# Kernel optimization log

Hardware: AMD Instinct MI355X
Metric: run time of the kernel (lower is better)

The kernel has to match this reference:

```python
import jax, jax.numpy as jnp
import numpy as np

K_SIZE = 3
NUM_HEADS = 8
DIM = 128        # per-head feature dim
R = 128          # sketch dim
BATCH = 2
LENGTH = 2048
OUT_DIM = DIM * NUM_HEADS


def _conv1d(x, w, b=None):
    # x: [B, Cin, L], w: [Cout, Cin, K]
    y = jax.lax.conv_general_dilated(x, w, window_strides=(1,), padding='VALID',
                                     dimension_numbers=('NCH', 'OIH', 'NCH'))
    if b is not None:
        y = y + b[None, :, None]
    return y


def _sketch(x, g1, g2):
    # p == 2 branch: Sx = sqrt(r) * tanh((x@G1)*(x@G2)/sqrt(r))
    sqrt_r = jnp.asarray(np.sqrt(R), x.dtype)
    return sqrt_r * jnp.tanh((x @ g1) * (x @ g2) / sqrt_r)


def setup_inputs() -> dict:
    key = jax.random.key(0)
    ks = jax.random.split(key, 12)
    inp = {
        'x': jax.random.normal(ks[0], (BATCH, DIM, LENGTH), jnp.float32),
        'q_w': jax.random.normal(ks[1], (OUT_DIM, DIM, K_SIZE), jnp.float32) * (1.0 / np.sqrt(DIM * K_SIZE)),
        'q_b': jnp.zeros((OUT_DIM,), jnp.float32),
        'k_w': jax.random.normal(ks[2], (OUT_DIM, DIM, K_SIZE), jnp.float32) * (1.0 / np.sqrt(DIM * K_SIZE)),
        'k_b': jnp.zeros((OUT_DIM,), jnp.float32),
        'v_w': jax.random.normal(ks[3], (OUT_DIM, DIM, 1), jnp.float32) * (1.0 / np.sqrt(DIM)),
        'g1_q': jax.random.normal(ks[4], (DIM, R), jnp.float32) * (1.0 / np.sqrt(R)),
        'g2_q': jax.random.normal(ks[5], (DIM, R), jnp.float32) * (1.0 / np.sqrt(R)),
        'g1_k': jax.random.normal(ks[6], (DIM, R), jnp.float32) * (1.0 / np.sqrt(R)),
        'g2_k': jax.random.normal(ks[7], (DIM, R), jnp.float32) * (1.0 / np.sqrt(R)),
        'gamma_q': jnp.ones((1,), jnp.float32),
        'beta_q': jnp.zeros((1,), jnp.float32),
        'gamma_k': jnp.ones((1,), jnp.float32),
        'beta_k': jnp.zeros((1,), jnp.float32),
        'proj_w': jax.random.normal(ks[8], (DIM, OUT_DIM), jnp.float32) * (1.0 / np.sqrt(OUT_DIM)),
        'proj_b': jnp.zeros((DIM,), jnp.float32),
    }
    return inp


def reference(x, q_w, q_b, k_w, k_b, v_w, g1_q, g2_q, g1_k, g2_k,
              gamma_q, beta_q, gamma_k, beta_k, proj_w, proj_b):
    B, D, L = x.shape
    H = NUM_HEADS
    # causal left pad, then conv1d QKV projections
    x_pad = jnp.pad(x, ((0, 0), (0, 0), (K_SIZE - 1, 0)))
    q = _conv1d(x_pad, q_w, q_b)   # [B, H*D, L]
    k = _conv1d(x_pad, k_w, k_b)
    v = _conv1d(x, v_w)            # kernel size 1, no bias

    def shape(t):  # [B, H*D, L] -> [B, H, L, D]
        return t.reshape(B, H, D, L).transpose(0, 1, 3, 2)

    q, k, v = shape(q), shape(k), shape(v)
    q = gamma_q * q + beta_q
    k = gamma_k * k + beta_k
    phi_q = _sketch(q, g1_q, g2_q)  # [B, H, L, R]
    phi_k = _sketch(k, g1_k, g2_k)
    scores = jnp.einsum('bhlr,bhmr->bhlm', phi_q, phi_k)  # [B, H, L, L]
    attn = scores / (jnp.sum(scores, axis=-1, keepdims=True) + 1e-6)
    o = jnp.einsum('bhlm,bhmd->bhld', attn, v)            # [B, H, L, D]
    o = o.transpose(0, 1, 3, 2).reshape(B, H * D, L).transpose(0, 2, 1)  # [B, L, H*D]
    return o @ proj_w.T + proj_b
```

## Files before the change

kernel.cpp:

```cpp
#include <hip/hip_runtime.h>
#include <math.h>

#define BB 2
#define DD 128
#define LL 2048
#define HH 8
#define OC 1024
#define RR_ 128
#define BL (BB*LL)
#define NROW (BL*HH)
#define XROWS 2052


typedef __bf16  bf16x8  __attribute__((ext_vector_type(8)));
typedef float   float4v __attribute__((ext_vector_type(4)));

__device__ __forceinline__ void enc2(const float* src, bf16x8& p1, bf16x8& p2) {
    #pragma unroll
    for (int j = 0; j < 8; ++j) {
        float v = src[j];
        __bf16 h1 = (__bf16)v;
        p1[j] = h1;
        p2[j] = (__bf16)(v - (float)h1);
    }
}

__device__ __forceinline__ float fast_phi(double u1, double u2) {
    const double TWO_ISR = 0.17677669529663688110;
    const double LOG2E   = 1.44269504088896340736;
    const double SR      = 11.313708498984760390;
    double y = (u1*u2) * (TWO_ISR * LOG2E);
    y = fmin(fmax(y, -1020.4), 1020.4);
    double n = rint(y);
    double f = y - n;
    float ff = (float)f;
    float q;
    q = fmaf(1.01780860092396960e-7f, ff, 1.32154867901443094e-6f);
    q = fmaf(q, ff, 1.52527338040598403e-5f);
    q = fmaf(q, ff, 1.54035303933816099e-4f);
    q = fmaf(q, ff, 1.33335581464284434e-3f);
    q = fmaf(q, ff, 9.61812910762847716e-3f);
    q = fmaf(q, ff, 5.55041086648215800e-2f);
    double t2   = fma(f, (double)q, 0.24022650695910071233);
    double head = fma(f, 0.69314718055994530942, 1.0);
    double E0   = fma(f*f, t2, head);
    int ni = (int)n;
    double En = __hiloint2double((ni + 1023) << 20, 0);
    double E  = E0 * En;
    double den = E + 1.0;
    double r = (double)__builtin_amdgcn_rcpf((float)den);
    r = r * fma(-den, r, 2.0);
    r = r * fma(-den, r, 2.0);
    double t = fma(-2.0, r, 1.0);
    return (float)(SR * t);
}

__global__ __launch_bounds__(256) void enc_fused_k(
    const float* __restrict__ q_w, const float* __restrict__ k_w,
    const float* __restrict__ v_w, const float* __restrict__ pw,
    const float* __restrict__ g1_q, const float* __restrict__ g2_q,
    const float* __restrict__ g1_k, const float* __restrict__ g2_k,
    const float* __restrict__ x,
    __bf16* __restrict__ wenc, __bf16* __restrict__ genc,
    __bf16* __restrict__ venc, __bf16* __restrict__ penc,
    __bf16* __restrict__ xenc)
{
    __shared__ float t[32][33];
    const int bid = blockIdx.x;
    const int tid = threadIdx.x;
    if (bid < 2304) {
        const int gid = bid*256 + tid;
        if (gid < 262144) {
            const int o = gid >> 7, c = gid & 127;
            #pragma unroll
            for (int tt = 0; tt < 3; ++tt) {
                float v = (o < 1024) ? q_w[(o*128 + c)*3 + tt]
                                     : k_w[((o-1024)*128 + c)*3 + tt];
                __bf16 h1 = (__bf16)v;  float r1 = v - (float)h1;
                __bf16 h2 = (__bf16)r1; float r2 = r1 - (float)h2;
                __bf16 h3 = (__bf16)r2;
                wenc[((size_t)(0*3 + tt)*2048 + o)*128 + c] = h1;
                wenc[((size_t)(1*3 + tt)*2048 + o)*128 + c] = h2;
                wenc[((size_t)(2*3 + tt)*2048 + o)*128 + c] = h3;
            }
        } else if (gid < 262144 + 65536) {
            const int g = gid - 262144;
            const int mat = g >> 14, rem = g & 16383;
            const int r = rem >> 7, d = rem & 127;
            const float* src = (mat == 0) ? g1_q : (mat == 1) ? g2_q
                             : (mat == 2) ? g1_k : g2_k;
            float v = src[d*RR_ + r];
            __bf16 h1 = (__bf16)v;  float r1 = v - (float)h1;
            __bf16 h2 = (__bf16)r1; float r2 = r1 - (float)h2;
            __bf16 h3 = (__bf16)r2;
            genc[((size_t)(mat*3 + 0)*128 + r)*128 + d] = h1;
            genc[((size_t)(mat*3 + 1)*128 + r)*128 + d] = h2;
            genc[((size_t)(mat*3 + 2)*128 + r)*128 + d] = h3;
        } else if (gid < 262144 + 65536 + 131072) {
            const int g = gid - 262144 - 65536;
            const int o = g >> 7, c = g & 127;
            float v = v_w[o*128 + c];
            __bf16 h1 = (__bf16)v;  float r1 = v - (float)h1;
            __bf16 h2 = (__bf16)r1;
            venc[((size_t)0*1024 + o)*128 + c] = h1;
            venc[((size_t)1*1024 + o)*128 + c] = h2;
        } else if (gid < 262144 + 65536 + 131072 + 131072) {
            const int g = gid - 262144 - 65536 - 131072;
            const int j = g >> 10, k = g & 1023;
            float v = pw[(size_t)j*OC + k];
            __bf16 h1 = (__bf16)v;  float r1 = v - (float)h1;
            __bf16 h2 = (__bf16)r1;
            penc[((size_t)(0*128 + j))*OC + k] = h1;
            penc[((size_t)(1*128 + j))*OC + k] = h2;
        }
    } else {
        const int g = bid - 2304;
        const int lt = g & 63, ct = (g >> 6) & 3, b = g >> 8;
        const int l0 = lt*32, c0 = ct*32;
        for (int e = tid; e < 32*32; e += 256) {
            int c = e >> 5, l = e & 31;
            t[c][l] = x[((size_t)(b*DD + c0 + c))*LL + l0 + l];
        }
        __syncthreads();
        for (int e = tid; e < 32*32; e += 256) {
            int l = e >> 5, c = e & 31;
            float v = t[c][l];
            __bf16 h1 = (__bf16)v;  float r1 = v - (float)h1;
            __bf16 h2 = (__bf16)r1; float r2 = r1 - (float)h2;
            __bf16 h3 = (__bf16)r2;
            const size_t row = (size_t)(l0 + l + 2);
            xenc[((size_t)(0*2 + b)*XROWS + row)*128 + c0 + c] = h1;
            xenc[((size_t)(1*2 + b)*XROWS + row)*128 + c0 + c] = h2;
            xenc[((size_t)(2*2 + b)*XROWS + row)*128 + c0 + c] = h3;
        }
        if (lt == 0 && ct == 0) {
            for (int e = tid; e < 2*128; e += 256) {
                int row = e >> 7, c = e & 127;
                xenc[((size_t)(0*2 + b)*XROWS + row)*128 + c] = (__bf16)0.f;
                xenc[((size_t)(1*2 + b)*XROWS + row)*128 + c] = (__bf16)0.f;
                xenc[((size_t)(2*2 + b)*XROWS + row)*128 + c] = (__bf16)0.f;
            }
        }
    }
}

__global__ __launch_bounds__(256, 3) void conv_mfma_k(
    const __bf16* __restrict__ xenc, const __bf16* __restrict__ wenc,
    const __bf16* __restrict__ venc,
    const float* __restrict__ q_b, const float* __restrict__ k_b,
    const float* __restrict__ gamma_q, const float* __restrict__ beta_q,
    const float* __restrict__ gamma_k, const float* __restrict__ beta_k,
    float* __restrict__ q_s, float* __restrict__ k_s, float* __restrict__ v_s)
{
    __shared__ __bf16 As[3][66][136];
    const int tid  = threadIdx.x;
    const int wave = tid >> 6;
    const int lane = tid & 63;
    const int m    = lane & 15;
    const int quad = lane >> 4;
    const int bx = blockIdx.x;
    const int b  = bx >> 5;
    const int lb0 = (bx & 31) << 6;
    const int yt = blockIdx.y;

    for (int e = tid; e < 3*66*16; e += 256) {
        const int p = e / (66*16), rem = e % (66*16);
        const int row = rem >> 4, cg = rem & 15;
        *(bf16x8*)&As[p][row][cg*8] =
            *(const bf16x8*)&xenc[((size_t)(p*2 + b)*XROWS + lb0 + row)*128 + cg*8];
    }
    __syncthreads();

    if (yt < 32) {
        const int o0 = yt << 6;
        const int osub = o0 + wave*16;
        float4v corr[4][2];
        float4v accm[4];
        double  s64[4][4];
        #pragma unroll
        for (int lt = 0; lt < 4; ++lt) {
            corr[lt][0] = (float4v){0.f,0.f,0.f,0.f};
            corr[lt][1] = (float4v){0.f,0.f,0.f,0.f};
            #pragma unroll
            for (int reg = 0; reg < 4; ++reg) s64[lt][reg] = 0.0;
        }
        #pragma unroll
        for (int cidx = 0; cidx < 4; ++cidx) {
            const int c0 = cidx << 5;
            #pragma unroll
            for (int lt = 0; lt < 4; ++lt) accm[lt] = (float4v){0.f,0.f,0.f,0.f};
            #pragma unroll
            for (int t = 0; t < 3; ++t) {
                size_t base = ((size_t)t*2048 + osub + m)*128 + c0 + quad*8;
                bf16x8 B1 = *(const bf16x8*)&wenc[base];
                bf16x8 B2 = *(const bf16x8*)&wenc[base + (size_t)3*2048*128];
                bf16x8 B3 = *(const bf16x8*)&wenc[base + (size_t)6*2048*128];
                #pragma unroll
                for (int lt = 0; lt < 4; ++lt) {
                    const int row = lt*16 + m + t;
                    bf16x8 A1 = *(const bf16x8*)&As[0][row][c0 + quad*8];
                    bf16x8 A2 = *(const bf16x8*)&As[1][row][c0 + quad*8];
                    bf16x8 A3 = *(const bf16x8*)&As[2][row][c0 + quad*8];
                    accm[lt]    = __builtin_amdgcn_mfma_f32_16x16x32_bf16(A1, B1, accm[lt], 0, 0, 0);
                    corr[lt][0] = __builtin_amdgcn_mfma_f32_16x16x32_bf16(A1, B2, corr[lt][0], 0, 0, 0);
                    corr[lt][1] = __builtin_amdgcn_mfma_f32_16x16x32_bf16(A2, B1, corr[lt][1], 0, 0, 0);
                    corr[lt][0] = __builtin_amdgcn_mfma_f32_16x16x32_bf16(A1, B3, corr[lt][0], 0, 0, 0);
                    corr[lt][1] = __builtin_amdgcn_mfma_f32_16x16x32_bf16(A3, B1, corr[lt][1], 0, 0, 0);
                    corr[lt][0] = __builtin_amdgcn_mfma_f32_16x16x32_bf16(A2, B2, corr[lt][0], 0, 0, 0);
                }
            }
            #pragma unroll
            for (int lt = 0; lt < 4; ++lt)
                #pragma unroll
                for (int reg = 0; reg < 4; ++reg)
                    s64[lt][reg] += (double)accm[lt][reg];
        }
        const int is_k = (o0 >= 1024);
        const double g  = (double)(is_k ? gamma_k[0] : gamma_q[0]);
        const double be = (double)(is_k ? beta_k[0]  : beta_q[0]);
        const int o_global = osub + m;
        const int o_local  = o_global - (is_k ? 1024 : 0);
        const double bias  = (double)(is_k ? k_b[o_local] : q_b[o_local]);
        float* dest = is_k ? k_s : q_s;
        #pragma unroll
        for (int lt = 0; lt < 4; ++lt) {
            #pragma unroll
            for (int reg = 0; reg < 4; ++reg) {
                double s = (double)corr[lt][0][reg] + (double)corr[lt][1][reg]
                         + s64[lt][reg];
                const int l = lb0 + lt*16 + quad*4 + reg;
                dest[((size_t)(b*LL + l))*OC + o_local] = (float)(g*(s + bias) + be);
            }
        }
    } else {
        const int o0 = (yt - 32) << 6;
        const int osub = o0 + wave*16;
        float4v corr[4];
        float4v accm[4];
        double  sv[4][4];
        #pragma unroll
        for (int lt = 0; lt < 4; ++lt) {
            corr[lt] = (float4v){0.f,0.f,0.f,0.f};
            #pragma unroll
            for (int reg = 0; reg < 4; ++reg) sv[lt][reg] = 0.0;
        }
        #pragma unroll
        for (int cidx = 0; cidx < 4; ++cidx) {
            const int c0 = cidx << 5;
            #pragma unroll
            for (int lt = 0; lt < 4; ++lt) accm[lt] = (float4v){0.f,0.f,0.f,0.f};
            size_t base = ((size_t)(osub + m))*128 + c0 + quad*8;
            bf16x8 B1 = *(const bf16x8*)&venc[base];
            bf16x8 B2 = *(const bf16x8*)&venc[base + (size_t)1024*128];
            #pragma unroll
            for (int lt = 0; lt < 4; ++lt) {
                const int row = lt*16 + m + 2;
                bf16x8 A1 = *(const bf16x8*)&As[0][row][c0 + quad*8];
                bf16x8 A2 = *(const bf16x8*)&As[1][row][c0 + quad*8];
                accm[lt] = __builtin_amdgcn_mfma_f32_16x16x32_bf16(A1, B1, accm[lt], 0, 0, 0);
                corr[lt] = __builtin_amdgcn_mfma_f32_16x16x32_bf16(A1, B2, corr[lt], 0, 0, 0);
                corr[lt] = __builtin_amdgcn_mfma_f32_16x16x32_bf16(A2, B1, corr[lt], 0, 0, 0);
                corr[lt] = __builtin_amdgcn_mfma_f32_16x16x32_bf16(A2, B2, corr[lt], 0, 0, 0);
            }
            #pragma unroll
            for (int lt = 0; lt < 4; ++lt)
                #pragma unroll
                for (int reg = 0; reg < 4; ++reg)
                    sv[lt][reg] += (double)accm[lt][reg];
        }
        const int o_local = osub + m;
        #pragma unroll
        for (int lt = 0; lt < 4; ++lt) {
            #pragma unroll
            for (int reg = 0; reg < 4; ++reg) {
                float s = (float)(sv[lt][reg] + (double)corr[lt][reg]);
                const int l = lb0 + lt*16 + quad*4 + reg;
                v_s[((size_t)(b*LL + l))*OC + o_local] = s;
            }
        }
    }
}

__global__ __launch_bounds__(256) void sketch_mfma_k(
    float* __restrict__ q_s, float* __restrict__ k_s,
    const __bf16* __restrict__ genc_all)
{
    __shared__ __bf16 As[3][32][136];
    const int tid  = threadIdx.x;
    const int wave = tid >> 6;
    const int lane = tid & 63;
    const int m    = lane & 15;
    const int quad = lane >> 4;
    const int half = blockIdx.x >> 10;
    float* buf = half ? k_s : q_s;
    const __bf16* genc = genc_all + (size_t)half*2*3*128*128;
    const size_t i0 = (size_t)(blockIdx.x & 1023) * 32;

    for (int e = tid; e < 32*32; e += 256) {
        const int row = e >> 5, d0 = (e & 31) << 2;
        const float4 v4 = *(const float4*)&buf[(i0 + row)*RR_ + d0];
        const float vs[4] = {v4.x, v4.y, v4.z, v4.w};
        #pragma unroll
        for (int j = 0; j < 4; ++j) {
            float v = vs[j];
            __bf16 h1 = (__bf16)v;  float r1 = v - (float)h1;
            __bf16 h2 = (__bf16)r1; float r2 = r1 - (float)h2;
            __bf16 h3 = (__bf16)r2;
            As[0][row][d0+j] = h1; As[1][row][d0+j] = h2; As[2][row][d0+j] = h3;
        }
    }
    __syncthreads();

    float4v accm[2][2][2], corr[2][2][2];
    #pragma unroll
    for (int mt = 0; mt < 2; ++mt)
        #pragma unroll
        for (int nt = 0; nt < 2; ++nt)
            #pragma unroll
            for (int mat = 0; mat < 2; ++mat) {
                accm[mt][nt][mat] = (float4v){0.f,0.f,0.f,0.f};
                corr[mt][nt][mat] = (float4v){0.f,0.f,0.f,0.f};
            }

    #pragma unroll
    for (int ck = 0; ck < 4; ++ck) {
        const int k0 = ck << 5;
        bf16x8 A1[2], A2[2], A3[2];
        #pragma unroll
        for (int mt = 0; mt < 2; ++mt) {
            A1[mt] = *(const bf16x8*)&As[0][mt*16 + m][k0 + quad*8];
            A2[mt] = *(const bf16x8*)&As[1][mt*16 + m][k0 + quad*8];
            A3[mt] = *(const bf16x8*)&As[2][mt*16 + m][k0 + quad*8];
        }
        #pragma unroll
        for (int nt = 0; nt < 2; ++nt) {
            const int r = wave*32 + nt*16 + m;
            #pragma unroll
            for (int mat = 0; mat < 2; ++mat) {
                size_t base = ((size_t)(mat*3)*128 + r)*128 + k0 + quad*8;
                bf16x8 B1 = *(const bf16x8*)&genc[base];
                bf16x8 B2 = *(const bf16x8*)&genc[base + (size_t)128*128];
                bf16x8 B3 = *(const bf16x8*)&genc[base + (size_t)2*128*128];
                #pragma unroll
                for (int mt = 0; mt < 2; ++mt) {
                    accm[mt][nt][mat] = __builtin_amdgcn_mfma_f32_16x16x32_bf16(A1[mt], B1, accm[mt][nt][mat], 0, 0, 0);
                    corr[mt][nt][mat] = __builtin_amdgcn_mfma_f32_16x16x32_bf16(A1[mt], B2, corr[mt][nt][mat], 0, 0, 0);
                    corr[mt][nt][mat] = __builtin_amdgcn_mfma_f32_16x16x32_bf16(A2[mt], B1, corr[mt][nt][mat], 0, 0, 0);
                    corr[mt][nt][mat] = __builtin_amdgcn_mfma_f32_16x16x32_bf16(A1[mt], B3, corr[mt][nt][mat], 0, 0, 0);
                    corr[mt][nt][mat] = __builtin_amdgcn_mfma_f32_16x16x32_bf16(A3[mt], B1, corr[mt][nt][mat], 0, 0, 0);
                    corr[mt][nt][mat] = __builtin_amdgcn_mfma_f32_16x16x32_bf16(A2[mt], B2, corr[mt][nt][mat], 0, 0, 0);
                }
            }
        }
    }
    __syncthreads();

    #pragma unroll
    for (int mt = 0; mt < 2; ++mt)
        #pragma unroll
        for (int nt = 0; nt < 2; ++nt)
            #pragma unroll
            for (int reg = 0; reg < 4; ++reg) {
                double u1 = (double)accm[mt][nt][0][reg] + (double)corr[mt][nt][0][reg];
                double u2 = (double)accm[mt][nt][1][reg] + (double)corr[mt][nt][1][reg];
                const size_t row = i0 + mt*16 + quad*4 + reg;
                const int col = wave*32 + nt*16 + m;
                buf[row*RR_ + col] = fast_phi(u1, u2);
            }
}

__global__ __launch_bounds__(512) void kv_mfma_k(
    const float* __restrict__ phi_k, const float* __restrict__ v,
    float* __restrict__ part_kv, double* __restrict__ part_ks)
{
    __shared__ float Pt[128*36];
    __shared__ float Vt[128*36];
    __shared__ double ksred[512];
    const int tid  = threadIdx.x;
    const int wave = tid >> 6;
    const int lane = tid & 63;
    const int m    = lane & 15;
    const int quad = lane >> 4;
    const int split = blockIdx.x;
    const int bh    = blockIdx.y;
    const int b = bh >> 3, h = bh & 7;
    const int lbase = split * 128;
    const int dh = wave & 1;
    const int rq = wave >> 1;

    float4v accm[4][2], corr[4][2];
    #pragma unroll
    for (int mt = 0; mt < 4; ++mt)
        #pragma unroll
        for (int nt = 0; nt < 2; ++nt) {
            accm[mt][nt] = (float4v){0.f,0.f,0.f,0.f};
            corr[mt][nt] = (float4v){0.f,0.f,0.f,0.f};
        }
    double ks = 0.0;

    for (int ch = 0; ch < 4; ++ch) {
        __syncthreads();
        for (int e = tid; e < 32*128; e += 512) {
            const int l = e >> 7, r = e & 127;
            size_t base = ((size_t)(b*LL + lbase + ch*32 + l)*HH + h)*RR_;
            float pv = phi_k[base + r];
            float vv = v[base + r];
            Pt[r*36 + l] = pv;
            Vt[r*36 + l] = vv;
            ks += (double)pv;
        }
        __syncthreads();
        bf16x8 A1[4], A2[4], B1[2], B2[2];
        #pragma unroll
        for (int mt = 0; mt < 4; ++mt)
            enc2(&Vt[(dh*64 + mt*16 + m)*36 + quad*8], A1[mt], A2[mt]);
        #pragma unroll
        for (int nt = 0; nt < 2; ++nt)
            enc2(&Pt[(rq*32 + nt*16 + m)*36 + quad*8], B1[nt], B2[nt]);
        #pragma unroll
        for (int mt = 0; mt < 4; ++mt)
            #pragma unroll
            for (int nt = 0; nt < 2; ++nt) {
                accm[mt][nt] = __builtin_amdgcn_mfma_f32_16x16x32_bf16(A1[mt], B1[nt], accm[mt][nt], 0, 0, 0);
                corr[mt][nt] = __builtin_amdgcn_mfma_f32_16x16x32_bf16(A1[mt], B2[nt], corr[mt][nt], 0, 0, 0);
                corr[mt][nt] = __builtin_amdgcn_mfma_f32_16x16x32_bf16(A2[mt], B1[nt], corr[mt][nt], 0, 0, 0);
                corr[mt][nt] = __builtin_amdgcn_mfma_f32_16x16x32_bf16(A2[mt], B2[nt], corr[mt][nt], 0, 0, 0);
            }
    }

    ksred[tid] = ks;
    __syncthreads();
    if (tid < 128) {
        double s = ksred[tid] + ksred[tid+128] + ksred[tid+256] + ksred[tid+384];
        part_ks[(bh*16 + split)*RR_ + tid] = s;
    }

    float* outp = part_kv + ((size_t)(bh*16 + split))*RR_*DD;
    #pragma unroll
    for (int mt = 0; mt < 4; ++mt)
        #pragma unroll
        for (int nt = 0; nt < 2; ++nt)
            #pragma unroll
            for (int reg = 0; reg < 4; ++reg) {
                const int d = dh*64 + mt*16 + quad*4 + reg;
                const int r = rq*32 + nt*16 + m;
                outp[d*128 + r] = accm[mt][nt][reg] + corr[mt][nt][reg];
            }
}

__global__ __launch_bounds__(256) void kvreduce_k(
    const float* __restrict__ part_kv, __bf16* __restrict__ kvt_enc)
{
    const int gid = blockIdx.x*256 + threadIdx.x;
    if (gid >= 16*RR_*DD) return;
    const int bh = gid >> 14;
    const int rd = gid & 16383;
    float s = 0.f;
    #pragma unroll
    for (int c = 0; c < 16; ++c)
        s += part_kv[(((size_t)(bh*16 + c)) << 14) + rd];
    __bf16 h1 = (__bf16)s;
    __bf16 h2 = (__bf16)(s - (float)h1);
    kvt_enc[(size_t)bh*16384 + rd] = h1;
    kvt_enc[(size_t)(16 + bh)*16384 + rd] = h2;
}

__global__ __launch_bounds__(256) void numden_mfma_k(
    const float* __restrict__ phi_q, const __bf16* __restrict__ kvt_enc,
    const double* __restrict__ part_ks, float* __restrict__ o_out)
{
    __shared__ float Pq[64*132];
    __shared__ double Ks_s[128];
    __shared__ double den_s[64];
    const int tid  = threadIdx.x;
    const int wave = tid >> 6;
    const int lane = tid & 63;
    const int m    = lane & 15;
    const int quad = lane >> 4;
    const int lt = blockIdx.x;
    const int bh = blockIdx.y;
    const int b = bh >> 3, h = bh & 7;
    const int l0 = lt * 64;

    if (tid < 128) {
        double s = 0.0;
        #pragma unroll
        for (int c = 0; c < 16; ++c) s += part_ks[(bh*16 + c)*RR_ + tid];
        Ks_s[tid] = s;
    }
    for (int e = tid; e < 64*32; e += 256) {
        const int l = e >> 5, r0 = (e & 31) << 2;
        *(float4*)&Pq[l*132 + r0] =
            *(const float4*)&phi_q[((size_t)(b*LL + l0 + l)*HH + h)*RR_ + r0];
    }
    __syncthreads();

    double den = 0.0;
    if (tid < 64) {
        #pragma unroll
        for (int r = 0; r < 128; ++r)
            den += (double)Pq[tid*132 + r] * Ks_s[r];
    }

    float4v accm[4][2], corr[4][2];
    #pragma unroll
    for (int mt = 0; mt < 4; ++mt)
        #pragma unroll
        for (int nt = 0; nt < 2; ++nt) {
            accm[mt][nt] = (float4v){0.f,0.f,0.f,0.f};
            corr[mt][nt] = (float4v){0.f,0.f,0.f,0.f};
        }

    #pragma unroll
    for (int ck = 0; ck < 4; ++ck) {
        const int k0 = ck << 5;
        bf16x8 A1[4], A2[4];
        #pragma unroll
        for (int mt = 0; mt < 4; ++mt)
            enc2(&Pq[(mt*16 + m)*132 + k0 + quad*8], A1[mt], A2[mt]);
        #pragma unroll
        for (int nt = 0; nt < 2; ++nt) {
            const int d = wave*32 + nt*16 + m;
            size_t base = ((size_t)bh*128 + d)*128 + k0 + quad*8;
            bf16x8 B1 = *(const bf16x8*)&kvt_enc[base];
            bf16x8 B2 = *(const bf16x8*)&kvt_enc[base + (size_t)16*16384];
            #pragma unroll
            for (int mt = 0; mt < 4; ++mt) {
                accm[mt][nt] = __builtin_amdgcn_mfma_f32_16x16x32_bf16(A1[mt], B1, accm[mt][nt], 0, 0, 0);
                corr[mt][nt] = __builtin_amdgcn_mfma_f32_16x16x32_bf16(A1[mt], B2, corr[mt][nt], 0, 0, 0);
                corr[mt][nt] = __builtin_amdgcn_mfma_f32_16x16x32_bf16(A2[mt], B1, corr[mt][nt], 0, 0, 0);
                corr[mt][nt] = __builtin_amdgcn_mfma_f32_16x16x32_bf16(A2[mt], B2, corr[mt][nt], 0, 0, 0);
            }
        }
    }

    __syncthreads();
    if (tid < 64) den_s[tid] = den;
    __syncthreads();

    #pragma unroll
    for (int mt = 0; mt < 4; ++mt)
        #pragma unroll
        for (int nt = 0; nt < 2; ++nt)
            #pragma unroll
            for (int reg = 0; reg < 4; ++reg) {
                const int ll = mt*16 + quad*4 + reg;
                const int d  = wave*32 + nt*16 + m;
                const float inv = (float)(1.0 / (den_s[ll] + 1e-6));
                o_out[((size_t)(b*LL + l0 + ll))*OC + h*DD + d] =
                    (accm[mt][nt][reg] + corr[mt][nt][reg]) * inv;
            }
}

__global__ __launch_bounds__(256) void proj_part_mfma_k(
    const float* __restrict__ o_s, const __bf16* __restrict__ penc,
    float* __restrict__ part)
{
    __shared__ float As[32*260];
    const int tid  = threadIdx.x;
    const int wave = tid >> 6;
    const int lane = tid & 63;
    const int m    = lane & 15;
    const int quad = lane >> 4;
    const int row0  = blockIdx.x * 32;
    const int kbase = blockIdx.y * 256;

    for (int e = tid; e < 32*64; e += 256) {
        const int row = e >> 6, k0 = (e & 63) << 2;
        *(float4*)&As[row*260 + k0] =
            *(const float4*)&o_s[(size_t)(row0 + row)*OC + kbase + k0];
    }
    __syncthreads();

    float4v accm[2][2], corr[2][2];
    #pragma unroll
    for (int mt = 0; mt < 2; ++mt)
        #pragma unroll
        for (int nt = 0; nt < 2; ++nt) {
            accm[mt][nt] = (float4v){0.f,0.f,0.f,0.f};
            corr[mt][nt] = (float4v){0.f,0.f,0.f,0.f};
        }

    #pragma unroll
    for (int ck = 0; ck < 8; ++ck) {
        const int k0 = ck << 5;
        bf16x8 A1[2], A2[2];
        #pragma unroll
        for (int mt = 0; mt < 2; ++mt)
            enc2(&As[(mt*16 + m)*260 + k0 + quad*8], A1[mt], A2[mt]);
        #pragma unroll
        for (int nt = 0; nt < 2; ++nt) {
            const int j = wave*32 + nt*16 + m;
            size_t base = ((size_t)j)*OC + kbase + k0 + quad*8;
            bf16x8 B1 = *(const bf16x8*)&penc[base];
            bf16x8 B2 = *(const bf16x8*)&penc[base + (size_t)128*OC];
            #pragma unroll
            for (int mt = 0; mt < 2; ++mt) {
                accm[mt][nt] = __builtin_amdgcn_mfma_f32_16x16x32_bf16(A1[mt], B1, accm[mt][nt], 0, 0, 0);
                corr[mt][nt] = __builtin_amdgcn_mfma_f32_16x16x32_bf16(A1[mt], B2, corr[mt][nt], 0, 0, 0);
                corr[mt][nt] = __builtin_amdgcn_mfma_f32_16x16x32_bf16(A2[mt], B1, corr[mt][nt], 0, 0, 0);
                corr[mt][nt] = __builtin_amdgcn_mfma_f32_16x16x32_bf16(A2[mt], B2, corr[mt][nt], 0, 0, 0);
            }
        }
    }

    float* outp = part + (size_t)blockIdx.y*BL*DD;
    #pragma unroll
    for (int mt = 0; mt < 2; ++mt)
        #pragma unroll
        for (int nt = 0; nt < 2; ++nt)
            #pragma unroll
            for (int reg = 0; reg < 4; ++reg) {
                const int row = row0 + mt*16 + quad*4 + reg;
                const int j   = wave*32 + nt*16 + m;
                outp[(size_t)row*DD + j] = accm[mt][nt][reg] + corr[mt][nt][reg];
            }
}

__global__ __launch_bounds__(256) void proj_reduce_k(
    const float* __restrict__ part, const float* __restrict__ pb,
    float* __restrict__ out)
{
    const int gid = blockIdx.x*256 + threadIdx.x;
    if (gid >= BL*DD/4) return;
    const float4* p4 = (const float4*)part;
    float4 s = p4[gid];
    #pragma unroll
    for (int c = 1; c < 4; ++c) {
        float4 t = p4[gid + (size_t)c*(BL*DD/4)];
        s.x += t.x; s.y += t.y; s.z += t.z; s.w += t.w;
    }
    const int col = (gid << 2) & (DD-1);
    s.x += pb[col]; s.y += pb[col+1]; s.z += pb[col+2]; s.w += pb[col+3];
    ((float4*)out)[gid] = s;
}

extern "C" void kernel_launch(void* const* d_in, const int* in_sizes, int n_in,
                              void* d_out, int out_size, void* d_ws, size_t ws_size,
                              hipStream_t stream) {
    const float* x       = (const float*)d_in[0];
    const float* q_w     = (const float*)d_in[1];
    const float* q_b     = (const float*)d_in[2];
    const float* k_w     = (const float*)d_in[3];
    const float* k_b     = (const float*)d_in[4];
    const float* v_w     = (const float*)d_in[5];
    const float* g1_q    = (const float*)d_in[6];
    const float* g2_q    = (const float*)d_in[7];
    const float* g1_k    = (const float*)d_in[8];
    const float* g2_k    = (const float*)d_in[9];
    const float* gamma_q = (const float*)d_in[10];
    const float* beta_q  = (const float*)d_in[11];
    const float* gamma_k = (const float*)d_in[12];
    const float* beta_k  = (const float*)d_in[13];
    const float* proj_w  = (const float*)d_in[14];
    const float* proj_b  = (const float*)d_in[15];

    float* f = (float*)d_ws;
    float* q_s     = f;
    float* k_s     = f + 4194304;
    float* v_s     = f + 8388608;
    float* part_kv = f + 12582912;
    double* part_ks = (double*)(f + 16777216);
    __bf16* kvt_enc = (__bf16*)(f + 16842752);
    __bf16* genc   = (__bf16*)(f + 17104896);
    __bf16* venc   = (__bf16*)(f + 17203200);
    __bf16* penc   = (__bf16*)(f + 17334272);
    float* o_s     = k_s;
    float* proj_part = part_kv;
    __bf16* wenc   = (__bf16*)(f + 12582912);
    __bf16* xenc   = (__bf16*)(f + 13762560);

    dim3 blk(256);
    enc_fused_k<<<2816, blk, 0, stream>>>(q_w, k_w, v_w, proj_w,
                                          g1_q, g2_q, g1_k, g2_k, x,
                                          wenc, genc, venc, penc, xenc);
    conv_mfma_k<<<dim3(64,48), blk, 0, stream>>>(xenc, wenc, venc, q_b, k_b,
                                                 gamma_q, beta_q, gamma_k, beta_k,
                                                 q_s, k_s, v_s);
    sketch_mfma_k<<<2048, blk, 0, stream>>>(q_s, k_s, genc);
    kv_mfma_k<<<dim3(16,16), dim3(512), 0, stream>>>(k_s, v_s, part_kv, part_ks);
    kvreduce_k<<<1024, blk, 0, stream>>>(part_kv, kvt_enc);
    numden_mfma_k<<<dim3(32,16), blk, 0, stream>>>(q_s, kvt_enc, part_ks, o_s);
    proj_part_mfma_k<<<dim3(128,4), blk, 0, stream>>>(o_s, penc, proj_part);
    proj_reduce_k<<<512, blk, 0, stream>>>(proj_part, proj_b, (float*)d_out);
}
```

Baseline: 265.1 us.

## Double-buffer conv input tiles by channel chunk to cut LDS footprint

The conv kernel now stages the input tile in 32-channel chunks with two LDS buffers, prefetching the next chunk while computing the current one. This replaces a single large 3x66x136 tile, and the V branch loads only two precision planes. The smaller shared-memory footprint is meant to allow more resident blocks per CU and to overlap the staging loads with MFMA work, at the cost of an extra barrier per chunk. The sketch kernel also packs its three bf16 split components into 4-wide vector stores to LDS instead of scalar stores.

```diff
diff --git a/kernel.cpp b/kernel.cpp
--- a/kernel.cpp
+++ b/kernel.cpp
@@ -13,6 +13,7 @@
 
 
 typedef __bf16  bf16x8  __attribute__((ext_vector_type(8)));
+typedef __bf16  bf16x4  __attribute__((ext_vector_type(4)));
 typedef float   float4v __attribute__((ext_vector_type(4)));
 
 __device__ __forceinline__ void enc2(const float* src, bf16x8& p1, bf16x8& p2) {
@@ -152,7 +153,7 @@
     const float* __restrict__ gamma_k, const float* __restrict__ beta_k,
     float* __restrict__ q_s, float* __restrict__ k_s, float* __restrict__ v_s)
 {
-    __shared__ __bf16 As[3][66][136];
+    __shared__ __bf16 As[2][3][66][40];
     const int tid  = threadIdx.x;
     const int wave = tid >> 6;
     const int lane = tid & 63;
@@ -162,16 +163,18 @@
     const int b  = bx >> 5;
     const int lb0 = (bx & 31) << 6;
     const int yt = blockIdx.y;
-
-    for (int e = tid; e < 3*66*16; e += 256) {
-        const int p = e / (66*16), rem = e % (66*16);
-        const int row = rem >> 4, cg = rem & 15;
-        *(bf16x8*)&As[p][row][cg*8] =
+    const int is_conv = (yt < 32);
+    const int np = is_conv ? 3 : 2;
+
+    for (int e = tid; e < np*66*4; e += 256) {
+        const int p = e / (66*4), rem = e % (66*4);
+        const int row = rem >> 2, cg = rem & 3;
+        *(bf16x8*)&As[0][p][row][cg*8] =
             *(const bf16x8*)&xenc[((size_t)(p*2 + b)*XROWS + lb0 + row)*128 + cg*8];
     }
     __syncthreads();
 
-    if (yt < 32) {
+    if (is_conv) {
         const int o0 = yt << 6;
         const int osub = o0 + wave*16;
         float4v corr[4][2];
@@ -186,6 +189,16 @@
         }
         #pragma unroll
         for (int cidx = 0; cidx < 4; ++cidx) {
+            const int cur = cidx & 1;
+            if (cidx < 3) {
+                const int nc0 = (cidx + 1) << 5;
+                for (int e = tid; e < 3*66*4; e += 256) {
+                    const int p = e / (66*4), rem = e % (66*4);
+                    const int row = rem >> 2, cg = rem & 3;
+                    *(bf16x8*)&As[cur ^ 1][p][row][cg*8] =
+                        *(const bf16x8*)&xenc[((size_t)(p*2 + b)*XROWS + lb0 + row)*128 + nc0 + cg*8];
+                }
+            }
             const int c0 = cidx << 5;
             #pragma unroll
             for (int lt = 0; lt < 4; ++lt) accm[lt] = (float4v){0.f,0.f,0.f,0.f};
@@ -198,9 +211,9 @@
                 #pragma unroll
                 for (int lt = 0; lt < 4; ++lt) {
                     const int row = lt*16 + m + t;
-                    bf16x8 A1 = *(const bf16x8*)&As[0][row][c0 + quad*8];
-                    bf16x8 A2 = *(const bf16x8*)&As[1][row][c0 + quad*8];
-                    bf16x8 A3 = *(const bf16x8*)&As[2][row][c0 + quad*8];
+                    bf16x8 A1 = *(const bf16x8*)&As[cur][0][row][quad*8];
+                    bf16x8 A2 = *(const bf16x8*)&As[cur][1][row][quad*8];
+                    bf16x8 A3 = *(const bf16x8*)&As[cur][2][row][quad*8];
                     accm[lt]    = __builtin_amdgcn_mfma_f32_16x16x32_bf16(A1, B1, accm[lt], 0, 0, 0);
                     corr[lt][0] = __builtin_amdgcn_mfma_f32_16x16x32_bf16(A1, B2, corr[lt][0], 0, 0, 0);
                     corr[lt][1] = __builtin_amdgcn_mfma_f32_16x16x32_bf16(A2, B1, corr[lt][1], 0, 0, 0);
@@ -214,6 +227,7 @@
                 #pragma unroll
                 for (int reg = 0; reg < 4; ++reg)
                     s64[lt][reg] += (double)accm[lt][reg];
+            __syncthreads();
         }
         const int is_k = (o0 >= 1024);
         const double g  = (double)(is_k ? gamma_k[0] : gamma_q[0]);
@@ -246,6 +260,16 @@
         }
         #pragma unroll
         for (int cidx = 0; cidx < 4; ++cidx) {
+            const int cur = cidx & 1;
+            if (cidx < 3) {
+                const int nc0 = (cidx + 1) << 5;
+                for (int e = tid; e < 2*66*4; e += 256) {
+                    const int p = e / (66*4), rem = e % (66*4);
+                    const int row = rem >> 2, cg = rem & 3;
+                    *(bf16x8*)&As[cur ^ 1][p][row][cg*8] =
+                        *(const bf16x8*)&xenc[((size_t)(p*2 + b)*XROWS + lb0 + row)*128 + nc0 + cg*8];
+                }
+            }
             const int c0 = cidx << 5;
             #pragma unroll
             for (int lt = 0; lt < 4; ++lt) accm[lt] = (float4v){0.f,0.f,0.f,0.f};
@@ -255,8 +279,8 @@
             #pragma unroll
             for (int lt = 0; lt < 4; ++lt) {
                 const int row = lt*16 + m + 2;
-                bf16x8 A1 = *(const bf16x8*)&As[0][row][c0 + quad*8];
-                bf16x8 A2 = *(const bf16x8*)&As[1][row][c0 + quad*8];
+                bf16x8 A1 = *(const bf16x8*)&As[cur][0][row][quad*8];
+                bf16x8 A2 = *(const bf16x8*)&As[cur][1][row][quad*8];
                 accm[lt] = __builtin_amdgcn_mfma_f32_16x16x32_bf16(A1, B1, accm[lt], 0, 0, 0);
                 corr[lt] = __builtin_amdgcn_mfma_f32_16x16x32_bf16(A1, B2, corr[lt], 0, 0, 0);
                 corr[lt] = __builtin_amdgcn_mfma_f32_16x16x32_bf16(A2, B1, corr[lt], 0, 0, 0);
@@ -267,6 +291,7 @@
                 #pragma unroll
                 for (int reg = 0; reg < 4; ++reg)
                     sv[lt][reg] += (double)accm[lt][reg];
+            __syncthreads();
         }
         const int o_local = osub + m;
         #pragma unroll
@@ -300,14 +325,18 @@
         const int row = e >> 5, d0 = (e & 31) << 2;
         const float4 v4 = *(const float4*)&buf[(i0 + row)*RR_ + d0];
         const float vs[4] = {v4.x, v4.y, v4.z, v4.w};
+        bf16x4 o1, o2, o3;
         #pragma unroll
         for (int j = 0; j < 4; ++j) {
             float v = vs[j];
             __bf16 h1 = (__bf16)v;  float r1 = v - (float)h1;
             __bf16 h2 = (__bf16)r1; float r2 = r1 - (float)h2;
             __bf16 h3 = (__bf16)r2;
-            As[0][row][d0+j] = h1; As[1][row][d0+j] = h2; As[2][row][d0+j] = h3;
-        }
+            o1[j] = h1; o2[j] = h2; o3[j] = h3;
+        }
+        *(bf16x4*)&As[0][row][d0] = o1;
+        *(bf16x4*)&As[1][row][d0] = o2;
+        *(bf16x4*)&As[2][row][d0] = o3;
     }
     __syncthreads();
 
```

After: 255.2 us. -3.7%, faster.
